# Kernel tuning notes

Hardware: AMD Instinct MI355X
Metric: run time of the kernel (lower is better)

## Reference

```python
import jax, jax.numpy as jnp
import numpy as np


def setup_inputs() -> dict:
    key = jax.random.key(0)
    ks = jax.random.split(key, 14)
    N, D, H, L, K = 16384, 1024, 1024, 256, 4096
    s = 0.02  # small init scale for stable activations
    return {
        "x": jax.random.uniform(ks[0], (N, D), dtype=jnp.float32),
        "embed_pool": jax.random.normal(ks[1], (K, L), dtype=jnp.float32),
        "ew1": jax.random.normal(ks[2], (D, H), dtype=jnp.float32) * s,
        "eb1": jnp.zeros((H,), jnp.float32),
        "ew2": jax.random.normal(ks[3], (H, H), dtype=jnp.float32) * s,
        "eb2": jnp.zeros((H,), jnp.float32),
        "ew3": jax.random.normal(ks[4], (H, L), dtype=jnp.float32) * s,
        "eb3": jnp.zeros((L,), jnp.float32),
        "dw1": jax.random.normal(ks[5], (L, H), dtype=jnp.float32) * s,
        "db1": jnp.zeros((H,), jnp.float32),
        "dw2": jax.random.normal(ks[6], (H, H), dtype=jnp.float32) * s,
        "db2": jnp.zeros((H,), jnp.float32),
        "dw3": jax.random.normal(ks[7], (H, D), dtype=jnp.float32) * s,
        "db3": jnp.zeros((D,), jnp.float32),
    }


def _gelu(t):
    # torch nn.GELU default = exact erf gelu
    return jax.nn.gelu(t, approximate=False)


def reference(x, embed_pool, ew1, eb1, ew2, eb2, ew3, eb3, dw1, db1, dw2, db2, dw3, db3):
    sg = jax.lax.stop_gradient
    # encoder (Dropout is identity at eval)
    h = _gelu(x @ ew1 + eb1)
    h = _gelu(h @ ew2 + eb2)
    z_e = h @ ew3 + eb3  # [N, L]
    # vectorized nearest-neighbor codebook search (argmin of ||z_e - e_k||)
    # squared distances via expansion; argmin identical to argmin of norms
    d2 = (jnp.sum(z_e * z_e, axis=1, keepdims=True)
          - 2.0 * (z_e @ embed_pool.T)
          + jnp.sum(embed_pool * embed_pool, axis=1))  # [N, K]
    z_index = jnp.argmin(d2, axis=1)  # [N]
    z_discrete = jax.nn.one_hot(z_index, embed_pool.shape[0], dtype=jnp.int32)
    z_q = embed_pool[z_index]  # [N, L]
    # straight-through estimator
    z_ss = z_e - sg(z_e) + sg(z_q)
    # decoder
    h = _gelu(z_ss @ dw1 + db1)
    h = _gelu(h @ dw2 + db2)
    x_pred = jax.nn.sigmoid(h @ dw3 + db3)  # [N, D]
    loss = (jnp.sum((x - x_pred) ** 2)
            + jnp.sum((sg(z_e) - z_q) ** 2)
            + 0.25 * jnp.sum((z_e - sg(z_q)) ** 2)) / x.shape[0]
    return x_pred, z_discrete, loss
```

## Files before the change

kernel.cpp:

```cpp
#include <hip/hip_runtime.h>
#include <math.h>


#define MB (1024ULL * 1024ULL)

typedef __attribute__((ext_vector_type(8))) short s16x8;
typedef __attribute__((ext_vector_type(4))) float f32x4;

__device__ __forceinline__ ushort f2bf(float f) {
    unsigned u = __float_as_uint(f);
    u += 0x7fffu + ((u >> 16) & 1u);
    return (ushort)(u >> 16);
}
__device__ __forceinline__ float bf2f(ushort h) {
    return __uint_as_float(((unsigned)h) << 16);
}
__device__ __forceinline__ float gelu_f(float v) {
    return 0.5f * v * (1.0f + erff(v * 0.70710678118654752f));
}
__device__ __forceinline__ void gload16(const void* g, void* l) {
    __builtin_amdgcn_global_load_lds(
        (const __attribute__((address_space(1))) void*)g,
        (__attribute__((address_space(3))) void*)l, 16, 0, 0);
}

__device__ __forceinline__ void conv_body(const float* __restrict__ in,
                                          ushort* __restrict__ out,
                                          int n8, int vb, int nB)
{
    for (int i = vb * 256 + threadIdx.x; i < n8; i += nB * 256) {
        const float4 v0 = *(const float4*)(in + (size_t)i * 8);
        const float4 v1 = *(const float4*)(in + (size_t)i * 8 + 4);
        s16x8 h;
        h[0] = f2bf(v0.x); h[1] = f2bf(v0.y); h[2] = f2bf(v0.z); h[3] = f2bf(v0.w);
        h[4] = f2bf(v1.x); h[5] = f2bf(v1.y); h[6] = f2bf(v1.z); h[7] = f2bf(v1.w);
        *(s16x8*)(out + (size_t)i * 8) = h;
    }
}

__global__ __launch_bounds__(256)
void prep_all(const float* __restrict__ x, ushort* __restrict__ xb,
              const float* __restrict__ pool, ushort* __restrict__ poolb,
              float* __restrict__ cn,
              const float* __restrict__ ew1, ushort* __restrict__ w1,
              const float* __restrict__ ew2, ushort* __restrict__ w2,
              const float* __restrict__ ew3, ushort* __restrict__ w3,
              const float* __restrict__ dw1, ushort* __restrict__ v1,
              const float* __restrict__ dw2, ushort* __restrict__ v2,
              const float* __restrict__ dw3, ushort* __restrict__ v3)
{
    __shared__ float tile[32][33];
    const int b = blockIdx.x;
    const int tid = threadIdx.x;

    if (b < 2048) {
        conv_body(x, xb, 16384 * 1024 / 8, b, 2048);
        return;
    }
    if (b < 2560) {
        conv_body(pool, poolb, 4096 * 256 / 8, b - 2048, 512);
        return;
    }
    if (b < 3584) {
        const int r = (b - 2560) * 4 + (tid >> 6);
        const int lane = tid & 63;
        float4 v = *(const float4*)(pool + (size_t)r * 256 + lane * 4);
        float s = v.x * v.x + v.y * v.y + v.z * v.z + v.w * v.w;
        #pragma unroll
        for (int o = 32; o > 0; o >>= 1) s += __shfl_down(s, o);
        if (lane == 0) cn[r] = s;
        return;
    }

    const float* in; ushort* out; int Kd, Nn, vb;
    if (b < 4608)      { in = ew1; out = w1; Kd = 1024; Nn = 1024; vb = b - 3584; }
    else if (b < 5632) { in = ew2; out = w2; Kd = 1024; Nn = 1024; vb = b - 4608; }
    else if (b < 5888) { in = ew3; out = w3; Kd = 1024; Nn = 256;  vb = b - 5632; }
    else if (b < 6144) { in = dw1; out = v1; Kd = 256;  Nn = 1024; vb = b - 5888; }
    else if (b < 7168) { in = dw2; out = v2; Kd = 1024; Nn = 1024; vb = b - 6144; }
    else               { in = dw3; out = v3; Kd = 1024; Nn = 1024; vb = b - 7168; }

    const int nxw = Nn / 32;
    const int n0 = (vb % nxw) * 32, k0 = (vb / nxw) * 32;
    const int tx = tid & 31, ty = tid >> 5;
    #pragma unroll
    for (int r = 0; r < 4; r++)
        tile[ty + r * 8][tx] = in[(size_t)(k0 + ty + r * 8) * Nn + n0 + tx];
    __syncthreads();
    #pragma unroll
    for (int r = 0; r < 4; r++) {
        const float v = tile[tx][ty + r * 8];
        out[(size_t)(n0 + ty + r * 8) * Kd + k0 + tx] = f2bf(v);
    }
}

template<int EPI>
__global__ __launch_bounds__(512, 2)
void gemm_big(const ushort* __restrict__ A, const ushort* __restrict__ B,
              const float* __restrict__ bias, int Kd, int Nn,
              ushort* __restrict__ Cu, float* __restrict__ Cf,
              const float* __restrict__ xref, float* __restrict__ ssePartial,
              float* __restrict__ pval, int* __restrict__ pidx)
{
    extern __shared__ ushort smem[];
    constexpr int BUFS = 512 * 64;

    const int tid = threadIdx.x;
    const int wave = tid >> 6, lane = tid & 63;

    const int nx = gridDim.x;
    const int nwg = nx * gridDim.y;
    const int orig = blockIdx.y * nx + blockIdx.x;
    const int wgid = (orig & 7) * (nwg >> 3) + (orig >> 3);
    const int bx = wgid % nx, by = wgid / nx;

    const int m0 = by * 256, n0 = bx * 256;
    const int wr = wave >> 2, wc = wave & 3;
    const int fcol = lane & 15, kgrp = lane >> 4;
    const int NT = Kd / 64;
    const int rs = Kd * 2;

    const int srow = lane >> 3;
    const int sswz = ((lane & 7) ^ srow) << 4;
    const char* Abase = (const char*)A + (size_t)m0 * rs;
    const char* Bbase = (const char*)B + (size_t)n0 * rs;

    f32x4 acc[8][4];
    #pragma unroll
    for (int m = 0; m < 8; m++)
        #pragma unroll
        for (int n = 0; n < 4; n++)
            acc[m][n] = (f32x4){0.f, 0.f, 0.f, 0.f};

    auto STAGE = [&](int buf, int t) {
        ushort* dst = smem + buf * BUFS;
        const size_t kb = (size_t)t * 128;
        #pragma unroll
        for (int g = 0; g < 4; g++) {
            const int rb = g * 64 + wave * 8;
            gload16(Abase + (size_t)(rb + srow) * rs + kb + sswz, dst + rb * 64);
            gload16(Bbase + (size_t)(rb + srow) * rs + kb + sswz,
                    dst + (256 + rb) * 64);
        }
    };
    auto LD = [&](int buf, int r, int u) -> s16x8 {
        return *(const s16x8*)(smem + buf * BUFS + r * 64 + ((u ^ (r & 7)) << 3));
    };

    STAGE(0, 0);
    for (int t = 0; t < NT; ++t) {
        asm volatile("s_waitcnt vmcnt(0)" ::: "memory");
        __builtin_amdgcn_s_barrier();
        if (t + 1 < NT) STAGE((t + 1) & 1, t + 1);
        const int buf = t & 1;
        s16x8 b2[4][2];
        #pragma unroll
        for (int n = 0; n < 4; n++) {
            const int r = 256 + wc * 64 + n * 16 + fcol;
            #pragma unroll
            for (int ks = 0; ks < 2; ks++) b2[n][ks] = LD(buf, r, ks * 4 + kgrp);
        }
        #pragma unroll
        for (int h = 0; h < 2; h++) {
            s16x8 a2[4][2];
            #pragma unroll
            for (int i = 0; i < 4; i++) {
                const int r = wr * 128 + (h * 4 + i) * 16 + fcol;
                #pragma unroll
                for (int ks = 0; ks < 2; ks++) a2[i][ks] = LD(buf, r, ks * 4 + kgrp);
            }
            __builtin_amdgcn_s_setprio(1);
            #pragma unroll
            for (int i = 0; i < 4; i++)
                #pragma unroll
                for (int n = 0; n < 4; n++)
                    #pragma unroll
                    for (int ks = 0; ks < 2; ks++)
                        acc[h * 4 + i][n] = __builtin_amdgcn_mfma_f32_16x16x32_bf16(
                            a2[i][ks], b2[n][ks], acc[h * 4 + i][n], 0, 0, 0);
            __builtin_amdgcn_s_setprio(0);
        }
    }
    __builtin_amdgcn_sched_barrier(0);

    int colg[4];
    float bcol[4];
    #pragma unroll
    for (int n = 0; n < 4; n++) {
        colg[n] = n0 + wc * 64 + n * 16 + fcol;
        bcol[n] = bias[colg[n]];
    }

    if constexpr (EPI == 1) {
        #pragma unroll
        for (int m = 0; m < 8; m++)
            #pragma unroll
            for (int v = 0; v < 4; v++) {
                const int row = m0 + wr * 128 + m * 16 + kgrp * 4 + v;
                #pragma unroll
                for (int n = 0; n < 4; n++) {
                    float val = gelu_f(acc[m][n][v] + bcol[n]);
                    Cu[(size_t)row * Nn + colg[n]] = f2bf(val);
                }
            }
    } else if constexpr (EPI == 2) {
        float lsse = 0.0f;
        #pragma unroll
        for (int m = 0; m < 8; m++)
            #pragma unroll
            for (int v = 0; v < 4; v++) {
                const int row = m0 + wr * 128 + m * 16 + kgrp * 4 + v;
                const size_t rb = (size_t)row * Nn;
                #pragma unroll
                for (int n = 0; n < 4; n++) {
                    float val = acc[m][n][v] + bcol[n];
                    val = 1.0f / (1.0f + expf(-val));
                    __builtin_nontemporal_store(val, &Cf[rb + colg[n]]);
                    float d = xref[rb + colg[n]] - val;
                    lsse += d * d;
                }
            }
        __syncthreads();
        float* red = (float*)smem;
        red[tid] = lsse;
        __syncthreads();
        for (int s = 256; s > 0; s >>= 1) {
            if (tid < s) red[tid] += red[tid + s];
            __syncthreads();
        }
        if (tid == 0) ssePartial[by * nx + bx] = red[0];
    } else if constexpr (EPI == 3) {
        __syncthreads();
        float* sv = (float*)smem;
        int*   si = (int*)(sv + 1024);
        #pragma unroll
        for (int m = 0; m < 8; m++)
            #pragma unroll
            for (int v = 0; v < 4; v++) {
                float best = INFINITY;
                int bidx = 0x7fffffff;
                #pragma unroll
                for (int n = 0; n < 4; n++) {
                    float sc = bcol[n] - 2.0f * acc[m][n][v];
                    if (sc < best || (sc == best && colg[n] < bidx)) { best = sc; bidx = colg[n]; }
                }
                #pragma unroll
                for (int d = 1; d < 16; d <<= 1) {
                    float ov = __shfl_xor(best, d, 64);
                    int   oi = __shfl_xor(bidx, d, 64);
                    if (ov < best || (ov == best && oi < bidx)) { best = ov; bidx = oi; }
                }
                if (fcol == 0) {
                    const int rl = wr * 128 + m * 16 + kgrp * 4 + v;
                    sv[wc * 256 + rl] = best;
                    si[wc * 256 + rl] = bidx;
                }
            }
        __syncthreads();
        if (tid < 256) {
            float v0 = sv[tid];
            int   i0 = si[tid];
            #pragma unroll
            for (int c = 1; c < 4; c++) {
                float v1 = sv[c * 256 + tid];
                int   i1 = si[c * 256 + tid];
                if (v1 < v0 || (v1 == v0 && i1 < i0)) { v0 = v1; i0 = i1; }
            }
            pval[(size_t)(m0 + tid) * nx + bx] = v0;
            pidx[(size_t)(m0 + tid) * nx + bx] = i0;
        }
    }
}

__global__ __launch_bounds__(512, 2)
void gemm_enc3(const ushort* __restrict__ A, const ushort* __restrict__ B,
               const float* __restrict__ bias, int Kd, int Nn,
               ushort* __restrict__ Cu)
{
    extern __shared__ ushort smem[];
    constexpr int BUFS = 256 * 64;

    const int tid = threadIdx.x;
    const int wave = tid >> 6, lane = tid & 63;

    const int nx = gridDim.x;
    const int nwg = nx * gridDim.y;
    const int orig = blockIdx.y * nx + blockIdx.x;
    const int wgid = (orig & 7) * (nwg >> 3) + (orig >> 3);
    const int bx = wgid % nx, by = wgid / nx;

    const int m0 = by * 128, n0 = bx * 128;
    const int wr = wave >> 2, wc = wave & 3;
    const int fcol = lane & 15, kgrp = lane >> 4;
    const int NT = Kd / 64;
    const int rs = Kd * 2;

    const int srow = lane >> 3;
    const int sswz = ((lane & 7) ^ srow) << 4;
    const char* Abase = (const char*)A + (size_t)m0 * rs;
    const char* Bbase = (const char*)B + (size_t)n0 * rs;

    f32x4 acc[4][2];
    #pragma unroll
    for (int m = 0; m < 4; m++)
        #pragma unroll
        for (int n = 0; n < 2; n++)
            acc[m][n] = (f32x4){0.f, 0.f, 0.f, 0.f};

    auto STAGE = [&](int buf, int t) {
        ushort* dst = smem + buf * BUFS;
        const size_t kb = (size_t)t * 128;
        #pragma unroll
        for (int g = 0; g < 2; g++) {
            const int rb = g * 64 + wave * 8;
            gload16(Abase + (size_t)(rb + srow) * rs + kb + sswz, dst + rb * 64);
            gload16(Bbase + (size_t)(rb + srow) * rs + kb + sswz,
                    dst + (128 + rb) * 64);
        }
    };
    auto LD = [&](int buf, int r, int u) -> s16x8 {
        return *(const s16x8*)(smem + buf * BUFS + r * 64 + ((u ^ (r & 7)) << 3));
    };

    STAGE(0, 0);
    STAGE(1, 1);
    for (int t = 0; t < NT; ++t) {
        if (t + 1 < NT) asm volatile("s_waitcnt vmcnt(4)" ::: "memory");
        else            asm volatile("s_waitcnt vmcnt(0)" ::: "memory");
        __builtin_amdgcn_s_barrier();
        if (t + 2 < NT) STAGE((t + 2) % 3, t + 2);
        const int buf = t % 3;
        s16x8 a2[4][2], b2[2][2];
        #pragma unroll
        for (int m = 0; m < 4; m++) {
            const int r = wr * 64 + m * 16 + fcol;
            #pragma unroll
            for (int ks = 0; ks < 2; ks++) a2[m][ks] = LD(buf, r, ks * 4 + kgrp);
        }
        #pragma unroll
        for (int n = 0; n < 2; n++) {
            const int r = 128 + wc * 32 + n * 16 + fcol;
            #pragma unroll
            for (int ks = 0; ks < 2; ks++) b2[n][ks] = LD(buf, r, ks * 4 + kgrp);
        }
        __builtin_amdgcn_s_setprio(1);
        #pragma unroll
        for (int m = 0; m < 4; m++)
            #pragma unroll
            for (int n = 0; n < 2; n++)
                #pragma unroll
                for (int ks = 0; ks < 2; ks++)
                    acc[m][n] = __builtin_amdgcn_mfma_f32_16x16x32_bf16(
                        a2[m][ks], b2[n][ks], acc[m][n], 0, 0, 0);
        __builtin_amdgcn_s_setprio(0);
    }
    __builtin_amdgcn_sched_barrier(0);

    #pragma unroll
    for (int n = 0; n < 2; n++) {
        const int col = n0 + wc * 32 + n * 16 + fcol;
        const float bc = bias[col];
        #pragma unroll
        for (int m = 0; m < 4; m++)
            #pragma unroll
            for (int v = 0; v < 4; v++) {
                const int row = m0 + wr * 64 + m * 16 + kgrp * 4 + v;
                Cu[(size_t)row * Nn + col] = f2bf(acc[m][n][v] + bc);
            }
    }
}

__global__ __launch_bounds__(256)
void argmin_final(const float* __restrict__ pval, const int* __restrict__ pidx,
                  int nblk, const ushort* __restrict__ zE,
                  const float* __restrict__ pool,
                  float* __restrict__ zdisc, ushort* __restrict__ zq,
                  float* __restrict__ vqP)
{
    const int t = threadIdx.x;
    const int r = blockIdx.x * 4 + (t >> 6);
    const int l = t & 63;

    float best = INFINITY;
    int bi = 0x7fffffff;
    if (l < nblk) {
        best = pval[(size_t)r * nblk + l];
        bi = pidx[(size_t)r * nblk + l];
    }
    #pragma unroll
    for (int d = 32; d > 0; d >>= 1) {
        float ov = __shfl_xor(best, d, 64);
        int   oi = __shfl_xor(bi, d, 64);
        if (ov < best || (ov == best && oi < bi)) { best = ov; bi = oi; }
    }
    const int kbest = bi;

    f32x4* zrow = (f32x4*)(zdisc + (size_t)r * 4096);
    #pragma unroll
    for (int it = 0; it < 16; it++) {
        const int j = it * 64 + l;
        f32x4 o = (f32x4){0.f, 0.f, 0.f, 0.f};
        if ((kbest >> 2) == j) o[kbest & 3] = 1.0f;
        __builtin_nontemporal_store(o, &zrow[j]);
    }

    const float4 pz = *(const float4*)(pool + (size_t)kbest * 256 + l * 4);
    *(ushort4*)(zq + (size_t)r * 256 + l * 4) =
        make_ushort4(f2bf(pz.x), f2bf(pz.y), f2bf(pz.z), f2bf(pz.w));
    const ushort4 zh = *(const ushort4*)(zE + (size_t)r * 256 + l * 4);
    float d0 = bf2f(zh.x) - pz.x;
    float d1 = bf2f(zh.y) - pz.y;
    float d2 = bf2f(zh.z) - pz.z;
    float d3 = bf2f(zh.w) - pz.w;
    float s = d0 * d0 + d1 * d1 + d2 * d2 + d3 * d3;
    #pragma unroll
    for (int o = 32; o > 0; o >>= 1) s += __shfl_xor(s, o, 64);
    if (l == 0) vqP[r] = s;
}

__global__ __launch_bounds__(256)
void loss_final(const float* __restrict__ sseP, int nP,
                const float* __restrict__ vqP, int nV,
                float* __restrict__ out)
{
    int tid = threadIdx.x;
    float sx = 0.0f, svq = 0.0f;
    for (int i = tid; i < nP; i += 256) sx += sseP[i];
    for (int i = tid; i < nV; i += 256) svq += vqP[i];
    __shared__ float a[256], b[256];
    a[tid] = sx; b[tid] = svq;
    __syncthreads();
    for (int s = 128; s > 0; s >>= 1) {
        if (tid < s) { a[tid] += a[tid + s]; b[tid] += b[tid + s]; }
        __syncthreads();
    }
    if (tid == 0) out[0] = (a[0] + 1.25f * b[0]) / 16384.0f;
}

extern "C" void kernel_launch(void* const* d_in, const int* in_sizes, int n_in,
                              void* d_out, int out_size, void* d_ws, size_t ws_size,
                              hipStream_t stream)
{
    const float* x    = (const float*)d_in[0];
    const float* pool = (const float*)d_in[1];
    const float* ew1  = (const float*)d_in[2];
    const float* eb1  = (const float*)d_in[3];
    const float* ew2  = (const float*)d_in[4];
    const float* eb2  = (const float*)d_in[5];
    const float* ew3  = (const float*)d_in[6];
    const float* eb3  = (const float*)d_in[7];
    const float* dw1  = (const float*)d_in[8];
    const float* db1  = (const float*)d_in[9];
    const float* dw2  = (const float*)d_in[10];
    const float* db2  = (const float*)d_in[11];
    const float* dw3  = (const float*)d_in[12];
    const float* db3  = (const float*)d_in[13];

    const int N = 16384, D = 1024, H = 1024, L = 256, K = 4096;

    float* out   = (float*)d_out;
    float* xpred = out;
    float* zdisc = out + (size_t)N * D;
    float* lossp = zdisc + (size_t)N * K;

    char* ws = (char*)d_ws;
    ushort* xb    = (ushort*)(ws + 0 * MB);
    ushort* h1    = (ushort*)(ws + 32 * MB);
    ushort* h2    = (ushort*)(ws + 64 * MB);
    ushort* h3    = (ushort*)(ws + 96 * MB);
    ushort* h4    = (ushort*)(ws + 128 * MB);
    ushort* zE    = (ushort*)(ws + 160 * MB);
    ushort* zq    = (ushort*)(ws + 168 * MB);
    ushort* poolb = (ushort*)(ws + 176 * MB);
    ushort* w1    = (ushort*)(ws + 178 * MB);
    ushort* w2    = (ushort*)(ws + 180 * MB);
    ushort* w3    = (ushort*)(ws + 182 * MB);
    ushort* v1    = (ushort*)(ws + 183 * MB);
    ushort* v2    = (ushort*)(ws + 184 * MB);
    ushort* v3    = (ushort*)(ws + 186 * MB);
    float*  cn    = (float*)(ws + 188 * MB);
    float*  pv    = (float*)(ws + 189 * MB);
    int*    pi    = (int*)(ws + 190 * MB);
    float*  vqP   = (float*)(ws + 191 * MB);
    float*  sxP   = (float*)(ws + 192 * MB);

    const int SH_BIG = 2 * (512 * 64) * 2;
    const int SH_E3  = 3 * (256 * 64) * 2;
    (void)hipFuncSetAttribute((const void*)gemm_big<1>,
        hipFuncAttributeMaxDynamicSharedMemorySize, SH_BIG);
    (void)hipFuncSetAttribute((const void*)gemm_big<2>,
        hipFuncAttributeMaxDynamicSharedMemorySize, SH_BIG);
    (void)hipFuncSetAttribute((const void*)gemm_big<3>,
        hipFuncAttributeMaxDynamicSharedMemorySize, SH_BIG);
    (void)hipFuncSetAttribute((const void*)gemm_enc3,
        hipFuncAttributeMaxDynamicSharedMemorySize, SH_E3);

    dim3 blk(256), gblk(512);

    prep_all<<<8192, blk, 0, stream>>>(x, xb, pool, poolb, cn,
                                       ew1, w1, ew2, w2, ew3, w3,
                                       dw1, v1, dw2, v2, dw3, v3);

    gemm_big<1><<<dim3(H / 256, N / 256), gblk, SH_BIG, stream>>>(
        xb, w1, eb1, D, H, h1, nullptr, nullptr, nullptr, nullptr, nullptr);
    gemm_big<1><<<dim3(H / 256, N / 256), gblk, SH_BIG, stream>>>(
        h1, w2, eb2, H, H, h2, nullptr, nullptr, nullptr, nullptr, nullptr);
    gemm_enc3<<<dim3(L / 128, N / 128), gblk, SH_E3, stream>>>(
        h2, w3, eb3, H, L, zE);

    gemm_big<3><<<dim3(K / 256, N / 256), gblk, SH_BIG, stream>>>(
        zE, poolb, cn, L, K, nullptr, nullptr, nullptr, nullptr, pv, pi);

    argmin_final<<<N / 4, blk, 0, stream>>>(pv, pi, K / 256, zE, pool, zdisc, zq, vqP);

    gemm_big<1><<<dim3(H / 256, N / 256), gblk, SH_BIG, stream>>>(
        zq, v1, db1, L, H, h3, nullptr, nullptr, nullptr, nullptr, nullptr);
    gemm_big<1><<<dim3(H / 256, N / 256), gblk, SH_BIG, stream>>>(
        h3, v2, db2, H, H, h4, nullptr, nullptr, nullptr, nullptr, nullptr);
    gemm_big<2><<<dim3(D / 256, N / 256), gblk, SH_BIG, stream>>>(
        h4, v3, db3, H, D, nullptr, xpred, x, sxP, nullptr, nullptr);

    loss_final<<<1, blk, 0, stream>>>(sxP, (D / 256) * (N / 256), vqP, N, lossp);
}
```

Baseline: 413.2 us.

## Precompute decoder outputs per codebook entry and gather by argmin index

The decoder input is always one of the K=4096 codebook vectors, so the decoder MLP now runs once over the codebook (K rows) instead of over all N=16384 quantized rows. The per-row prediction is then gathered from the precomputed table, and the reconstruction SSE is computed in the gather kernel. This removes most of the decoder GEMM work at the cost of an extra fp32 table (K×D) and a gather pass. The decoder output is a function of the codebook weights only, not of a cached activation, so this is a legitimate algebraic reuse within a single call.

```diff
diff --git a/kernel.cpp b/kernel.cpp
--- a/kernel.cpp
+++ b/kernel.cpp
@@ -98,8 +98,7 @@
 __global__ __launch_bounds__(512, 2)
 void gemm_big(const ushort* __restrict__ A, const ushort* __restrict__ B,
               const float* __restrict__ bias, int Kd, int Nn,
-              ushort* __restrict__ Cu, float* __restrict__ Cf,
-              const float* __restrict__ xref, float* __restrict__ ssePartial,
+              ushort* __restrict__ Cu,
               float* __restrict__ pval, int* __restrict__ pidx)
 {
     extern __shared__ ushort smem[];
@@ -203,32 +202,6 @@
                     Cu[(size_t)row * Nn + colg[n]] = f2bf(val);
                 }
             }
-    } else if constexpr (EPI == 2) {
-        float lsse = 0.0f;
-        #pragma unroll
-        for (int m = 0; m < 8; m++)
-            #pragma unroll
-            for (int v = 0; v < 4; v++) {
-                const int row = m0 + wr * 128 + m * 16 + kgrp * 4 + v;
-                const size_t rb = (size_t)row * Nn;
-                #pragma unroll
-                for (int n = 0; n < 4; n++) {
-                    float val = acc[m][n][v] + bcol[n];
-                    val = 1.0f / (1.0f + expf(-val));
-                    __builtin_nontemporal_store(val, &Cf[rb + colg[n]]);
-                    float d = xref[rb + colg[n]] - val;
-                    lsse += d * d;
-                }
-            }
-        __syncthreads();
-        float* red = (float*)smem;
-        red[tid] = lsse;
-        __syncthreads();
-        for (int s = 256; s > 0; s >>= 1) {
-            if (tid < s) red[tid] += red[tid + s];
-            __syncthreads();
-        }
-        if (tid == 0) ssePartial[by * nx + bx] = red[0];
     } else if constexpr (EPI == 3) {
         __syncthreads();
         float* sv = (float*)smem;
@@ -272,10 +245,11 @@
     }
 }
 
+template<int EPI>
 __global__ __launch_bounds__(512, 2)
-void gemm_enc3(const ushort* __restrict__ A, const ushort* __restrict__ B,
-               const float* __restrict__ bias, int Kd, int Nn,
-               ushort* __restrict__ Cu)
+void gemm_128(const ushort* __restrict__ A, const ushort* __restrict__ B,
+              const float* __restrict__ bias, int Kd, int Nn,
+              ushort* __restrict__ Cu, float* __restrict__ Cf)
 {
     extern __shared__ ushort smem[];
     constexpr int BUFS = 256 * 64;
@@ -365,7 +339,14 @@
             #pragma unroll
             for (int v = 0; v < 4; v++) {
                 const int row = m0 + wr * 64 + m * 16 + kgrp * 4 + v;
-                Cu[(size_t)row * Nn + col] = f2bf(acc[m][n][v] + bc);
+                float val = acc[m][n][v] + bc;
+                if constexpr (EPI == 0) {
+                    Cu[(size_t)row * Nn + col] = f2bf(val);
+                } else if constexpr (EPI == 1) {
+                    Cu[(size_t)row * Nn + col] = f2bf(gelu_f(val));
+                } else {
+                    Cf[(size_t)row * Nn + col] = 1.0f / (1.0f + expf(-val));
+                }
             }
     }
 }
@@ -374,7 +355,7 @@
 void argmin_final(const float* __restrict__ pval, const int* __restrict__ pidx,
                   int nblk, const ushort* __restrict__ zE,
                   const float* __restrict__ pool,
-                  float* __restrict__ zdisc, ushort* __restrict__ zq,
+                  float* __restrict__ zdisc, int* __restrict__ kbo,
                   float* __restrict__ vqP)
 {
     const int t = threadIdx.x;
@@ -405,8 +386,6 @@
     }
 
     const float4 pz = *(const float4*)(pool + (size_t)kbest * 256 + l * 4);
-    *(ushort4*)(zq + (size_t)r * 256 + l * 4) =
-        make_ushort4(f2bf(pz.x), f2bf(pz.y), f2bf(pz.z), f2bf(pz.w));
     const ushort4 zh = *(const ushort4*)(zE + (size_t)r * 256 + l * 4);
     float d0 = bf2f(zh.x) - pz.x;
     float d1 = bf2f(zh.y) - pz.y;
@@ -415,7 +394,35 @@
     float s = d0 * d0 + d1 * d1 + d2 * d2 + d3 * d3;
     #pragma unroll
     for (int o = 32; o > 0; o >>= 1) s += __shfl_xor(s, o, 64);
-    if (l == 0) vqP[r] = s;
+    if (l == 0) { vqP[r] = s; kbo[r] = kbest; }
+}
+
+__global__ __launch_bounds__(256)
+void gather_pred(const int* __restrict__ kb, const float* __restrict__ xpT,
+                 const float* __restrict__ x, float* __restrict__ xpred,
+                 float* __restrict__ sseP)
+{
+    const int t = threadIdx.x;
+    const int r = blockIdx.x * 4 + (t >> 6);
+    const int l = t & 63;
+    const int k = kb[r];
+    const float* src = xpT + (size_t)k * 1024;
+    const float* xr  = x + (size_t)r * 1024;
+    float* dst = xpred + (size_t)r * 1024;
+    float s = 0.0f;
+    #pragma unroll
+    for (int j = 0; j < 4; j++) {
+        const int c = (j * 64 + l) * 4;
+        f32x4 v = *(const f32x4*)(src + c);
+        const float4 xv = *(const float4*)(xr + c);
+        __builtin_nontemporal_store(v, (f32x4*)(dst + c));
+        float d0 = xv.x - v[0], d1 = xv.y - v[1];
+        float d2 = xv.z - v[2], d3 = xv.w - v[3];
+        s += d0 * d0 + d1 * d1 + d2 * d2 + d3 * d3;
+    }
+    #pragma unroll
+    for (int o = 32; o > 0; o >>= 1) s += __shfl_xor(s, o, 64);
+    if (l == 0) sseP[r] = s;
 }
 
 __global__ __launch_bounds__(256)
@@ -467,33 +474,36 @@
     ushort* xb    = (ushort*)(ws + 0 * MB);
     ushort* h1    = (ushort*)(ws + 32 * MB);
     ushort* h2    = (ushort*)(ws + 64 * MB);
-    ushort* h3    = (ushort*)(ws + 96 * MB);
-    ushort* h4    = (ushort*)(ws + 128 * MB);
-    ushort* zE    = (ushort*)(ws + 160 * MB);
-    ushort* zq    = (ushort*)(ws + 168 * MB);
-    ushort* poolb = (ushort*)(ws + 176 * MB);
-    ushort* w1    = (ushort*)(ws + 178 * MB);
-    ushort* w2    = (ushort*)(ws + 180 * MB);
-    ushort* w3    = (ushort*)(ws + 182 * MB);
-    ushort* v1    = (ushort*)(ws + 183 * MB);
-    ushort* v2    = (ushort*)(ws + 184 * MB);
-    ushort* v3    = (ushort*)(ws + 186 * MB);
-    float*  cn    = (float*)(ws + 188 * MB);
-    float*  pv    = (float*)(ws + 189 * MB);
-    int*    pi    = (int*)(ws + 190 * MB);
-    float*  vqP   = (float*)(ws + 191 * MB);
-    float*  sxP   = (float*)(ws + 192 * MB);
+    ushort* zE    = (ushort*)(ws + 96 * MB);
+    ushort* poolb = (ushort*)(ws + 104 * MB);
+    ushort* w1    = (ushort*)(ws + 106 * MB);
+    ushort* w2    = (ushort*)(ws + 108 * MB);
+    ushort* w3    = (ushort*)(ws + 110 * MB);
+    ushort* v1    = (ushort*)(ws + 111 * MB);
+    ushort* v2    = (ushort*)(ws + 112 * MB);
+    ushort* v3    = (ushort*)(ws + 114 * MB);
+    ushort* t3    = (ushort*)(ws + 116 * MB);
+    ushort* t4    = (ushort*)(ws + 124 * MB);
+    float*  xpT   = (float*)(ws + 132 * MB);
+    float*  cn    = (float*)(ws + 148 * MB);
+    float*  pv    = (float*)(ws + 149 * MB);
+    int*    pi    = (int*)(ws + 150 * MB);
+    int*    kbo   = (int*)(ws + 151 * MB);
+    float*  vqP   = (float*)(ws + 152 * MB);
+    float*  sxP   = (float*)(ws + 153 * MB);
 
     const int SH_BIG = 2 * (512 * 64) * 2;
-    const int SH_E3  = 3 * (256 * 64) * 2;
+    const int SH_128 = 3 * (256 * 64) * 2;
     (void)hipFuncSetAttribute((const void*)gemm_big<1>,
-        hipFuncAttributeMaxDynamicSharedMemorySize, SH_BIG);
-    (void)hipFuncSetAttribute((const void*)gemm_big<2>,
         hipFuncAttributeMaxDynamicSharedMemorySize, SH_BIG);
     (void)hipFuncSetAttribute((const void*)gemm_big<3>,
         hipFuncAttributeMaxDynamicSharedMemorySize, SH_BIG);
-    (void)hipFuncSetAttribute((const void*)gemm_enc3,
-        hipFuncAttributeMaxDynamicSharedMemorySize, SH_E3);
+    (void)hipFuncSetAttribute((const void*)gemm_128<0>,
+        hipFuncAttributeMaxDynamicSharedMemorySize, SH_128);
+    (void)hipFuncSetAttribute((const void*)gemm_128<1>,
+        hipFuncAttributeMaxDynamicSharedMemorySize, SH_128);
+    (void)hipFuncSetAttribute((const void*)gemm_128<2>,
+        hipFuncAttributeMaxDynamicSharedMemorySize, SH_128);
 
     dim3 blk(256), gblk(512);
 
@@ -501,24 +511,26 @@
                                        ew1, w1, ew2, w2, ew3, w3,
                                        dw1, v1, dw2, v2, dw3, v3);
 
+    gemm_128<1><<<dim3(H / 128, K / 128), gblk, SH_128, stream>>>(
+        poolb, v1, db1, L, H, t3, nullptr);
+    gemm_128<1><<<dim3(H / 128, K / 128), gblk, SH_128, stream>>>(
+        t3, v2, db2, H, H, t4, nullptr);
+    gemm_128<2><<<dim3(D / 128, K / 128), gblk, SH_128, stream>>>(
+        t4, v3, db3, H, D, nullptr, xpT);
+
     gemm_big<1><<<dim3(H / 256, N / 256), gblk, SH_BIG, stream>>>(
-        xb, w1, eb1, D, H, h1, nullptr, nullptr, nullptr, nullptr, nullptr);
+        xb, w1, eb1, D, H, h1, nullptr, nullptr);
     gemm_big<1><<<dim3(H / 256, N / 256), gblk, SH_BIG, stream>>>(
-        h1, w2, eb2, H, H, h2, nullptr, nullptr, nullptr, nullptr, nullptr);
-    gemm_enc3<<<dim3(L / 128, N / 128), gblk, SH_E3, stream>>>(
-        h2, w3, eb3, H, L, zE);
+        h1, w2, eb2, H, H, h2, nullptr, nullptr);
+    gemm_128<0><<<dim3(L / 128, N / 128), gblk, SH_128, stream>>>(
+        h2, w3, eb3, H, L, zE, nullptr);
 
     gemm_big<3><<<dim3(K / 256, N / 256), gblk, SH_BIG, stream>>>(
-        zE, poolb, cn, L, K, nullptr, nullptr, nullptr, nullptr, pv, pi);
-
-    argmin_final<<<N / 4, blk, 0, stream>>>(pv, pi, K / 256, zE, pool, zdisc, zq, vqP);
-
-    gemm_big<1><<<dim3(H / 256, N / 256), gblk, SH_BIG, stream>>>(
-        zq, v1, db1, L, H, h3, nullptr, nullptr, nullptr, nullptr, nullptr);
-    gemm_big<1><<<dim3(H / 256, N / 256), gblk, SH_BIG, stream>>>(
-        h3, v2, db2, H, H, h4, nullptr, nullptr, nullptr, nullptr, nullptr);
-    gemm_big<2><<<dim3(D / 256, N / 256), gblk, SH_BIG, stream>>>(
-        h4, v3, db3, H, D, nullptr, xpred, x, sxP, nullptr, nullptr);
-
-    loss_final<<<1, blk, 0, stream>>>(sxP, (D / 256) * (N / 256), vqP, N, lossp);
-}
+        zE, poolb, cn, L, K, nullptr, pv, pi);
+
+    argmin_final<<<N / 4, blk, 0, stream>>>(pv, pi, K / 256, zE, pool, zdisc, kbo, vqP);
+
+    gather_pred<<<N / 4, blk, 0, stream>>>(kbo, xpT, x, xpred, sxP);
+
+    loss_final<<<1, blk, 0, stream>>>(sxP, N, vqP, N, lossp);
+}
```

Result: faster. 370.7 us (-10.3%).
